# Kernel tuning notes

Hardware: AMD Instinct MI355X
Metric: run time of the kernel (lower is better)

Reference implementation:

```python
import jax, jax.numpy as jnp
import numpy as np

B, S, D = 2, 2048, 1024
H = 16
HD = D // H

def setup_inputs() -> dict:
    key = jax.random.key(0)
    k1, k2, k3 = jax.random.split(key, 3)
    x = jax.random.normal(k1, (B, S, D), dtype=jnp.float32)
    w_attn = jax.random.normal(k2, (D, 3 * D), dtype=jnp.float32) * (1.0 / np.sqrt(D))
    b_attn = jnp.zeros((3 * D,), dtype=jnp.float32)
    w_proj = jax.random.normal(k3, (D, D), dtype=jnp.float32) * (1.0 / np.sqrt(D))
    b_proj = jnp.zeros((D,), dtype=jnp.float32)
    return {"x": x, "w_attn": w_attn, "b_attn": b_attn, "w_proj": w_proj, "b_proj": b_proj}

def reference(x, w_attn, b_attn, w_proj, b_proj):
    bsz, seq_len, embed_dim = x.shape
    qkv = x @ w_attn + b_attn                      # [B,S,3D]
    q, k, v = jnp.split(qkv, 3, axis=-1)
    # [B,S,D] -> [B,H,S,HD]
    def heads(t):
        return t.reshape(bsz, seq_len, H, HD).transpose(0, 2, 1, 3)
    q, k, v = heads(q), heads(k), heads(v)
    scale = 1.0 / np.sqrt(HD)
    att = jnp.einsum('bhqd,bhkd->bhqk', q, k) * scale  # [B,H,S,S]
    causal = jnp.tril(jnp.ones((seq_len, seq_len), dtype=bool))
    att = jnp.where(causal[None, None], att, jnp.float32(-jnp.inf))
    att = jax.nn.softmax(att, axis=-1)
    y = jnp.einsum('bhqk,bhkd->bhqd', att, v)          # [B,H,S,HD]
    y = y.transpose(0, 2, 1, 3).reshape(bsz, seq_len, embed_dim)
    return y @ w_proj + b_proj
```

## Files before the change

### kernel.cpp

```cpp
#include <hip/hip_runtime.h>
#include <hip/hip_bf16.h>
#include <math.h>

typedef __bf16 bf16x8 __attribute__((ext_vector_type(8)));
typedef __bf16 bf16x4 __attribute__((ext_vector_type(4)));
typedef float f32x4 __attribute__((ext_vector_type(4)));

#define LOG2E 1.44269504088896340736f

#define SEQ 2048
#define DMODEL 1024
#define NH 16
#define HD 64

__device__ __forceinline__ void gl2lds16(const void* g, void* l) {
  __builtin_amdgcn_global_load_lds((__attribute__((address_space(1))) void*)g,
                                   (__attribute__((address_space(3))) void*)l,
                                   16, 0, 0);
}

__device__ __forceinline__ unsigned compute_flag_local(const unsigned* __restrict__ x,
                                                       int* cnt) {
  int c = 0;
  for (int i = threadIdx.x; i < 4096; i += 256) {
    unsigned e = (x[i] >> 23) & 0xFF;
    c += (e >= 0x70 && e <= 0x8F) ? 1 : 0;
  }
#pragma unroll
  for (int o = 32; o > 0; o >>= 1) c += __shfl_xor(c, o, 64);
  if ((threadIdx.x & 63) == 0) cnt[threadIdx.x >> 6] = c;
  __syncthreads();
  const int tot = cnt[0] + cnt[1] + cnt[2] + cnt[3];
  return (tot > 2048) ? 1u : 0u;
}

__device__ __forceinline__ void transpose_tile(const void* __restrict__ in,
                                               __hip_bfloat16* __restrict__ out,
                                               int R, int C, int c0, int r0, bool f32,
                                               __hip_bfloat16 (*tile)[65]) {
  const int tx = threadIdx.x & 63, ty = threadIdx.x >> 6;
#pragma unroll
  for (int i = 0; i < 16; ++i) {
    int r = ty + i * 4;
    long idx = (long)(r0 + r) * C + c0 + tx;
    tile[r][tx] = f32 ? __float2bfloat16(((const float*)in)[idx])
                      : ((const __hip_bfloat16*)in)[idx];
  }
  __syncthreads();
#pragma unroll
  for (int i = 0; i < 16; ++i) {
    int r = ty + i * 4;
    out[(long)(c0 + r) * R + r0 + tx] = tile[tx][r];
  }
}

__global__ void prep_all(const void* __restrict__ x, const void* __restrict__ w_attn,
                         const void* __restrict__ w_proj,
                         __hip_bfloat16* __restrict__ x_bf,
                         __hip_bfloat16* __restrict__ wT_attn,
                         __hip_bfloat16* __restrict__ wT_proj,
                         unsigned* __restrict__ flag) {
  __shared__ int cnt[4];
  __shared__ __hip_bfloat16 tile[64][65];
  const unsigned f = compute_flag_local((const unsigned*)x, cnt);
  const int bid = blockIdx.x;
  if (bid == 0 && threadIdx.x == 0) flag[0] = f;

  if (bid < 1024) {
#pragma unroll
    for (int rep = 0; rep < 4; ++rep) {
      const int i = ((bid * 4 + rep) * 256 + threadIdx.x) * 4;
      if (f) {
        const float4 v = *(const float4*)((const float*)x + i);
        x_bf[i + 0] = __float2bfloat16(v.x);
        x_bf[i + 1] = __float2bfloat16(v.y);
        x_bf[i + 2] = __float2bfloat16(v.z);
        x_bf[i + 3] = __float2bfloat16(v.w);
      } else {
        *(bf16x4*)(x_bf + i) = *(const bf16x4*)((const __hip_bfloat16*)x + i);
      }
    }
  } else if (bid < 1024 + 768) {
    const int b2 = bid - 1024;
    const int c0 = (b2 % 48) * 64, r0 = (b2 / 48) * 64;
    transpose_tile(w_attn, wT_attn, 1024, 3072, c0, r0, f != 0, tile);
  } else {
    const int b3 = bid - 1024 - 768;
    const int c0 = (b3 % 16) * 64, r0 = (b3 / 16) * 64;
    transpose_tile(w_proj, wT_proj, 1024, 1024, c0, r0, f != 0, tile);
  }
}

template <int MODE, int BN>
__global__ __launch_bounds__(256, BN == 128 ? 3 : 6) void gemm_bt(
    const __hip_bfloat16* __restrict__ A, const __hip_bfloat16* __restrict__ Bt,
    const void* __restrict__ bias, void* __restrict__ C,
    __hip_bfloat16* __restrict__ q_ws, __hip_bfloat16* __restrict__ k_ws,
    __hip_bfloat16* __restrict__ vt_ws, int M, int N, int K,
    const unsigned* __restrict__ flag) {
  constexpr int NJ = BN / 32;
  alignas(16) __shared__ __hip_bfloat16 lA[128 * 64];
  alignas(16) __shared__ __hip_bfloat16 lB[BN * 64];
  const int tid = threadIdx.x;
  const int wave = tid >> 6, lane = tid & 63;
  const int l15 = lane & 15, lq = lane >> 4;
  const int m0 = blockIdx.y * 128, n0 = blockIdx.x * BN;
  const int wrow = (wave >> 1) * 64, wcol = (wave & 1) * (BN / 2);

  const int rs = lane >> 3;
  const int cs = lane & 7;
  const int gch = cs ^ rs;
  const __hip_bfloat16* ap0 = A + (long)(m0 + wave * 32 + rs) * K + gch * 8;
  const __hip_bfloat16* bp0 = Bt + (long)(n0 + wave * (BN / 4) + rs) * K + gch * 8;

  f32x4 acc[4][NJ];
#pragma unroll
  for (int i = 0; i < 4; ++i)
#pragma unroll
    for (int j = 0; j < NJ; ++j) acc[i][j] = {0.f, 0.f, 0.f, 0.f};

  for (int k0 = 0; k0 < K; k0 += 64) {
    __syncthreads();
#pragma unroll
    for (int i = 0; i < 4; ++i)
      gl2lds16(ap0 + (long)(i * 8) * K + k0, lA + (wave * 4 + i) * 512);
#pragma unroll
    for (int i = 0; i < NJ; ++i)
      gl2lds16(bp0 + (long)(i * 8) * K + k0, lB + (wave * NJ + i) * 512);
    __syncthreads();
#pragma unroll
    for (int ks = 0; ks < 2; ++ks) {
      bf16x8 af[4], bfr[NJ];
#pragma unroll
      for (int i = 0; i < 4; ++i) {
        const int p = wrow + 16 * i + l15;
        af[i] = *(const bf16x8*)(lA + p * 64 + (((ks * 4 + lq) ^ (l15 & 7)) * 8));
      }
#pragma unroll
      for (int j = 0; j < NJ; ++j) {
        const int p = wcol + 16 * j + l15;
        bfr[j] = *(const bf16x8*)(lB + p * 64 + (((ks * 4 + lq) ^ (l15 & 7)) * 8));
      }
#pragma unroll
      for (int i = 0; i < 4; ++i)
#pragma unroll
        for (int j = 0; j < NJ; ++j)
          acc[i][j] = __builtin_amdgcn_mfma_f32_16x16x32_bf16(af[i], bfr[j], acc[i][j], 0, 0, 0);
    }
  }

  const bool f32in = (*flag != 0);
  const bool outf32 = (MODE == 0) && f32in;
  const float KSCL = 0.125f * LOG2E;
#pragma unroll
  for (int i = 0; i < 4; ++i) {
    const int row = m0 + wrow + 16 * i + lq * 4;
#pragma unroll
    for (int j = 0; j < NJ; ++j) {
      const int col = n0 + wcol + 16 * j + l15;
      const float bv = f32in ? ((const float*)bias)[col]
                             : __bfloat162float(((const __hip_bfloat16*)bias)[col]);
#pragma unroll
      for (int r = 0; r < 4; ++r) {
        const float v = acc[i][j][r] + bv;
        const int rr = row + r;
        if (MODE == 0) {
          if (outf32)
            ((float*)C)[(long)rr * N + col] = v;
          else
            ((__hip_bfloat16*)C)[(long)rr * N + col] = __float2bfloat16(v);
        } else {
          const int which = col >> 10;
          const int f = col & 1023;
          const int h = f >> 6, d = f & 63;
          const int b = rr >> 11, s = rr & 2047;
          const long bh = (long)b * NH + h;
          if (which == 0)
            q_ws[(bh * SEQ + s) * HD + d] = __float2bfloat16(v);
          else if (which == 1)
            k_ws[(bh * SEQ + s) * HD + d] = __float2bfloat16(v * KSCL);
          else {
            const int w = s & 31;
            const int wl = w & 15;
            const int sig = (w >> 4) ? (2 * (wl & ~3) + 4 + (wl & 3))
                                     : (2 * (wl & ~3) + (wl & 3));
            const int sp = (s & ~31) | sig;
            vt_ws[(bh * HD + d) * SEQ + sp] = __float2bfloat16(v);
          }
        }
      }
    }
  }
}

__global__ __launch_bounds__(256, 5) void attn_fused(
    const __hip_bfloat16* __restrict__ q_ws, const __hip_bfloat16* __restrict__ k_ws,
    const __hip_bfloat16* __restrict__ vt_ws, __hip_bfloat16* __restrict__ y_ws) {
  alignas(16) __shared__ __hip_bfloat16 lK[2][64 * 64];
  alignas(16) __shared__ __hip_bfloat16 lV[2][64 * 64];
  const int tid = threadIdx.x, wave = tid >> 6, lane = tid & 63;
  const int l15 = lane & 15, lq = lane >> 4;
  const int grp = blockIdx.x >> 5;
  const int bh = blockIdx.x & 31;
  const int gg = grp & 7, qq = grp >> 3;
  const int qt = (qq == 0) ? (31 - gg)
               : (qq == 1) ? (16 + gg)
               : (qq == 2) ? (15 - gg)
                           : gg;
  const int q0 = qt * 64;
  const int nkt = qt + 1;
  const __hip_bfloat16* Qb = q_ws + (long)bh * SEQ * HD;
  const __hip_bfloat16* Kb = k_ws + (long)bh * SEQ * HD;
  const __hip_bfloat16* Vb = vt_ws + (long)bh * HD * SEQ;
  const int b = bh >> 4, h = bh & 15;

  const int qrow = q0 + wave * 16 + l15;
  const bf16x8 qa0 = *(const bf16x8*)(Qb + (long)qrow * HD + lq * 8);
  const bf16x8 qa1 = *(const bf16x8*)(Qb + (long)qrow * HD + 32 + lq * 8);

  f32x4 accO[4];
  f32x4 accL;
#pragma unroll
  for (int j = 0; j < 4; ++j) accO[j] = {0.f, 0.f, 0.f, 0.f};
  accL = {0.f, 0.f, 0.f, 0.f};
  const __bf16 one = (__bf16)1.0f;
  const bf16x8 onesA = {one, one, one, one, one, one, one, one};

  const int p0 = wave * 16 + (lane >> 3);
  const int cl = lane & 7;
  const __hip_bfloat16* kpre[2];
  const __hip_bfloat16* vpre[2];

#pragma unroll
  for (int i = 0; i < 2; ++i) {
    const int p = p0 + i * 8;
    const int c = cl ^ (p & 7);
    kpre[i] = Kb + (long)p * HD + c * 8;
    vpre[i] = Vb + (long)p * SEQ + c * 8;
    gl2lds16(kpre[i], &lK[0][(wave * 16 + i * 8) * 64]);
    gl2lds16(vpre[i], &lV[0][(wave * 16 + i * 8) * 64]);
    kpre[i] += 64 * HD;
    vpre[i] += 64;
  }

#pragma unroll 1
  for (int kt = 0; kt < nkt; ++kt) {
    const int buf = kt & 1;
    if (kt + 1 < nkt) {
#pragma unroll
      for (int i = 0; i < 2; ++i) {
        gl2lds16(kpre[i], &lK[buf ^ 1][(wave * 16 + i * 8) * 64]);
        gl2lds16(vpre[i], &lV[buf ^ 1][(wave * 16 + i * 8) * 64]);
        kpre[i] += 64 * HD;
        vpre[i] += 64;
      }
      asm volatile("s_waitcnt vmcnt(4)\n\ts_barrier" ::: "memory");
    } else {
      asm volatile("s_waitcnt vmcnt(0)\n\ts_barrier" ::: "memory");
    }
    const __hip_bfloat16* lKb = lK[buf];
    const __hip_bfloat16* lVb = lV[buf];

    f32x4 st[4];
    __builtin_amdgcn_s_setprio(1);
#pragma unroll
    for (int t = 0; t < 4; ++t) {
      st[t] = {0.f, 0.f, 0.f, 0.f};
      const int pp = t * 16 + l15;
      const bf16x8 kb0 = *(const bf16x8*)(lKb + (pp * 8 + (lq ^ (pp & 7))) * 8);
      const bf16x8 kb1 = *(const bf16x8*)(lKb + (pp * 8 + ((4 + lq) ^ (pp & 7))) * 8);
      st[t] = __builtin_amdgcn_mfma_f32_16x16x32_bf16(kb0, qa0, st[t], 0, 0, 0);
      st[t] = __builtin_amdgcn_mfma_f32_16x16x32_bf16(kb1, qa1, st[t], 0, 0, 0);
    }
    __builtin_amdgcn_s_setprio(0);

    const bool diag = (kt == nkt - 1);
    const int qloc = wave * 16 + l15;
    bf16x8 pb[2];
#pragma unroll
    for (int c = 0; c < 2; ++c) {
#pragma unroll
      for (int t2 = 0; t2 < 2; ++t2) {
        const int tt = c * 2 + t2;
#pragma unroll
        for (int r = 0; r < 4; ++r) {
          float pv = exp2f(st[tt][r]);
          if (diag) {
            const int colloc = tt * 16 + lq * 4 + r;
            pv = (colloc <= qloc) ? pv : 0.f;
          }
          pb[c][t2 * 4 + r] = (__bf16)pv;
        }
      }
    }

    __builtin_amdgcn_s_setprio(1);
#pragma unroll
    for (int j = 0; j < 4; ++j) {
      const int d = j * 16 + l15;
      const bf16x8 va0 = *(const bf16x8*)(lVb + (d * 8 + (lq ^ (d & 7))) * 8);
      const bf16x8 va1 = *(const bf16x8*)(lVb + (d * 8 + ((4 + lq) ^ (d & 7))) * 8);
      accO[j] = __builtin_amdgcn_mfma_f32_16x16x32_bf16(va0, pb[0], accO[j], 0, 0, 0);
      accO[j] = __builtin_amdgcn_mfma_f32_16x16x32_bf16(va1, pb[1], accO[j], 0, 0, 0);
    }
    accL = __builtin_amdgcn_mfma_f32_16x16x32_bf16(onesA, pb[0], accL, 0, 0, 0);
    accL = __builtin_amdgcn_mfma_f32_16x16x32_bf16(onesA, pb[1], accL, 0, 0, 0);
    __builtin_amdgcn_s_setprio(0);
    asm volatile("s_barrier" ::: "memory");
  }

  const float inv = 1.f / accL[0];
  const int s = q0 + wave * 16 + l15;
  __hip_bfloat16* yb = y_ws + (long)(b * SEQ + s) * DMODEL + h * HD;
#pragma unroll
  for (int j = 0; j < 4; ++j) {
    bf16x4 o;
#pragma unroll
    for (int r = 0; r < 4; ++r) o[r] = (__bf16)(accO[j][r] * inv);
    *(bf16x4*)(yb + j * 16 + lq * 4) = o;
  }
}

extern "C" void kernel_launch(void* const* d_in, const int* in_sizes, int n_in,
                              void* d_out, int out_size, void* d_ws, size_t ws_size,
                              hipStream_t stream) {
  const void* x = d_in[0];
  const void* w_attn = d_in[1];
  const void* b_attn = d_in[2];
  const void* w_proj = d_in[3];
  const void* b_proj = d_in[4];

  char* ws = (char*)d_ws;
  const size_t MB = 1024 * 1024;
  unsigned* flag = (unsigned*)ws;
  __hip_bfloat16* wT_attn = (__hip_bfloat16*)(ws + 1 * MB);
  __hip_bfloat16* wT_proj = (__hip_bfloat16*)(ws + 7 * MB);
  __hip_bfloat16* x_bf = (__hip_bfloat16*)(ws + 9 * MB);
  __hip_bfloat16* q_ws = (__hip_bfloat16*)(ws + 17 * MB);
  __hip_bfloat16* k_ws = (__hip_bfloat16*)(ws + 25 * MB);
  __hip_bfloat16* vt_ws = (__hip_bfloat16*)(ws + 33 * MB);
  __hip_bfloat16* y_ws = (__hip_bfloat16*)(ws + 41 * MB);

  prep_all<<<dim3(1024 + 768 + 256), 256, 0, stream>>>(
      x, w_attn, w_proj, x_bf, wT_attn, wT_proj, flag);

  gemm_bt<1, 64><<<dim3(3072 / 64, 4096 / 128), 256, 0, stream>>>(
      x_bf, wT_attn, b_attn, nullptr, q_ws, k_ws, vt_ws, 4096, 3072, 1024, flag);

  attn_fused<<<dim3(1024), 256, 0, stream>>>(q_ws, k_ws, vt_ws, y_ws);

  gemm_bt<0, 64><<<dim3(1024 / 64, 4096 / 128), 256, 0, stream>>>(
      y_ws, wT_proj, b_proj, d_out, nullptr, nullptr, nullptr, 4096, 1024, 1024, flag);
}
```

Measured before the change: 192.2 us.

## Split attention tile 2x2 across waves over query and key halves with LDS reduction

Each wave now handles 32 query rows and 32 key columns of the 64x64 tile instead of 16 query rows against all 64 keys. Each K fragment and V fragment read from LDS is reused across two query fragments, which halves the per-wave LDS reads for K and V. Partial outputs and row sums from the two key-half waves are combined at the end through LDS with an extra sync. The cost is more accumulator registers (8 output tiles instead of 4), which may pressure the occupancy target of 5, plus the final reduction step.

Result: faster. 185.7 us (-3.4%).

```diff
diff --git a/kernel.cpp b/kernel.cpp
--- a/kernel.cpp
+++ b/kernel.cpp
@@ -200,6 +200,7 @@
   alignas(16) __shared__ __hip_bfloat16 lV[2][64 * 64];
   const int tid = threadIdx.x, wave = tid >> 6, lane = tid & 63;
   const int l15 = lane & 15, lq = lane >> 4;
+  const int qh = wave & 1, kh = wave >> 1;
   const int grp = blockIdx.x >> 5;
   const int bh = blockIdx.x & 31;
   const int gg = grp & 7, qq = grp >> 3;
@@ -214,15 +215,23 @@
   const __hip_bfloat16* Vb = vt_ws + (long)bh * HD * SEQ;
   const int b = bh >> 4, h = bh & 15;
 
-  const int qrow = q0 + wave * 16 + l15;
-  const bf16x8 qa0 = *(const bf16x8*)(Qb + (long)qrow * HD + lq * 8);
-  const bf16x8 qa1 = *(const bf16x8*)(Qb + (long)qrow * HD + 32 + lq * 8);
-
-  f32x4 accO[4];
-  f32x4 accL;
-#pragma unroll
-  for (int j = 0; j < 4; ++j) accO[j] = {0.f, 0.f, 0.f, 0.f};
-  accL = {0.f, 0.f, 0.f, 0.f};
+  bf16x8 qa[2][2];
+#pragma unroll
+  for (int qf = 0; qf < 2; ++qf) {
+    const int qrow = q0 + qh * 32 + qf * 16 + l15;
+#pragma unroll
+    for (int ks = 0; ks < 2; ++ks)
+      qa[qf][ks] = *(const bf16x8*)(Qb + (long)qrow * HD + ks * 32 + lq * 8);
+  }
+
+  f32x4 accO[4][2];
+  f32x4 accL[2];
+#pragma unroll
+  for (int df = 0; df < 4; ++df)
+#pragma unroll
+    for (int qf = 0; qf < 2; ++qf) accO[df][qf] = {0.f, 0.f, 0.f, 0.f};
+  accL[0] = {0.f, 0.f, 0.f, 0.f};
+  accL[1] = {0.f, 0.f, 0.f, 0.f};
   const __bf16 one = (__bf16)1.0f;
   const bf16x8 onesA = {one, one, one, one, one, one, one, one};
 
@@ -261,63 +270,93 @@
     const __hip_bfloat16* lKb = lK[buf];
     const __hip_bfloat16* lVb = lV[buf];
 
-    f32x4 st[4];
+    f32x4 st[2][2];
     __builtin_amdgcn_s_setprio(1);
 #pragma unroll
-    for (int t = 0; t < 4; ++t) {
-      st[t] = {0.f, 0.f, 0.f, 0.f};
-      const int pp = t * 16 + l15;
+    for (int kf = 0; kf < 2; ++kf) {
+      const int pp = kh * 32 + kf * 16 + l15;
       const bf16x8 kb0 = *(const bf16x8*)(lKb + (pp * 8 + (lq ^ (pp & 7))) * 8);
       const bf16x8 kb1 = *(const bf16x8*)(lKb + (pp * 8 + ((4 + lq) ^ (pp & 7))) * 8);
-      st[t] = __builtin_amdgcn_mfma_f32_16x16x32_bf16(kb0, qa0, st[t], 0, 0, 0);
-      st[t] = __builtin_amdgcn_mfma_f32_16x16x32_bf16(kb1, qa1, st[t], 0, 0, 0);
+#pragma unroll
+      for (int qf = 0; qf < 2; ++qf) {
+        st[kf][qf] = {0.f, 0.f, 0.f, 0.f};
+        st[kf][qf] = __builtin_amdgcn_mfma_f32_16x16x32_bf16(kb0, qa[qf][0], st[kf][qf], 0, 0, 0);
+        st[kf][qf] = __builtin_amdgcn_mfma_f32_16x16x32_bf16(kb1, qa[qf][1], st[kf][qf], 0, 0, 0);
+      }
     }
     __builtin_amdgcn_s_setprio(0);
 
     const bool diag = (kt == nkt - 1);
-    const int qloc = wave * 16 + l15;
     bf16x8 pb[2];
 #pragma unroll
-    for (int c = 0; c < 2; ++c) {
-#pragma unroll
-      for (int t2 = 0; t2 < 2; ++t2) {
-        const int tt = c * 2 + t2;
+    for (int qf = 0; qf < 2; ++qf) {
+      const int qloc = qh * 32 + qf * 16 + l15;
+#pragma unroll
+      for (int kf = 0; kf < 2; ++kf)
 #pragma unroll
         for (int r = 0; r < 4; ++r) {
-          float pv = exp2f(st[tt][r]);
+          float pv = exp2f(st[kf][qf][r]);
           if (diag) {
-            const int colloc = tt * 16 + lq * 4 + r;
+            const int colloc = kh * 32 + kf * 16 + lq * 4 + r;
             pv = (colloc <= qloc) ? pv : 0.f;
           }
-          pb[c][t2 * 4 + r] = (__bf16)pv;
+          pb[qf][kf * 4 + r] = (__bf16)pv;
         }
-      }
     }
 
     __builtin_amdgcn_s_setprio(1);
 #pragma unroll
-    for (int j = 0; j < 4; ++j) {
-      const int d = j * 16 + l15;
-      const bf16x8 va0 = *(const bf16x8*)(lVb + (d * 8 + (lq ^ (d & 7))) * 8);
-      const bf16x8 va1 = *(const bf16x8*)(lVb + (d * 8 + ((4 + lq) ^ (d & 7))) * 8);
-      accO[j] = __builtin_amdgcn_mfma_f32_16x16x32_bf16(va0, pb[0], accO[j], 0, 0, 0);
-      accO[j] = __builtin_amdgcn_mfma_f32_16x16x32_bf16(va1, pb[1], accO[j], 0, 0, 0);
-    }
-    accL = __builtin_amdgcn_mfma_f32_16x16x32_bf16(onesA, pb[0], accL, 0, 0, 0);
-    accL = __builtin_amdgcn_mfma_f32_16x16x32_bf16(onesA, pb[1], accL, 0, 0, 0);
+    for (int df = 0; df < 4; ++df) {
+      const int d = df * 16 + l15;
+      const bf16x8 va = *(const bf16x8*)(lVb + (d * 8 + ((kh * 4 + lq) ^ (d & 7))) * 8);
+#pragma unroll
+      for (int qf = 0; qf < 2; ++qf)
+        accO[df][qf] = __builtin_amdgcn_mfma_f32_16x16x32_bf16(va, pb[qf], accO[df][qf], 0, 0, 0);
+    }
+    accL[0] = __builtin_amdgcn_mfma_f32_16x16x32_bf16(onesA, pb[0], accL[0], 0, 0, 0);
+    accL[1] = __builtin_amdgcn_mfma_f32_16x16x32_bf16(onesA, pb[1], accL[1], 0, 0, 0);
     __builtin_amdgcn_s_setprio(0);
     asm volatile("s_barrier" ::: "memory");
   }
 
-  const float inv = 1.f / accL[0];
-  const int s = q0 + wave * 16 + l15;
-  __hip_bfloat16* yb = y_ws + (long)(b * SEQ + s) * DMODEL + h * HD;
-#pragma unroll
-  for (int j = 0; j < 4; ++j) {
-    bf16x4 o;
-#pragma unroll
-    for (int r = 0; r < 4; ++r) o[r] = (__bf16)(accO[j][r] * inv);
-    *(bf16x4*)(yb + j * 16 + lq * 4) = o;
+  {
+    float* red = (qh == 0) ? (float*)&lK[0][0] : (float*)&lV[0][0];
+    if (kh == 1) {
+#pragma unroll
+      for (int df = 0; df < 4; ++df)
+#pragma unroll
+        for (int qf = 0; qf < 2; ++qf)
+#pragma unroll
+          for (int r = 0; r < 4; ++r)
+            red[((df * 2 + qf) * 4 + r) * 64 + lane] = accO[df][qf][r];
+      red[32 * 64 + lane] = accL[0][0];
+      red[33 * 64 + lane] = accL[1][0];
+    }
+    __syncthreads();
+    if (kh == 0) {
+#pragma unroll
+      for (int df = 0; df < 4; ++df)
+#pragma unroll
+        for (int qf = 0; qf < 2; ++qf)
+#pragma unroll
+          for (int r = 0; r < 4; ++r)
+            accO[df][qf][r] += red[((df * 2 + qf) * 4 + r) * 64 + lane];
+      const float l0 = accL[0][0] + red[32 * 64 + lane];
+      const float l1 = accL[1][0] + red[33 * 64 + lane];
+#pragma unroll
+      for (int qf = 0; qf < 2; ++qf) {
+        const float inv = 1.f / (qf ? l1 : l0);
+        const int s = q0 + qh * 32 + qf * 16 + l15;
+        __hip_bfloat16* yb = y_ws + (long)(b * SEQ + s) * DMODEL + h * HD;
+#pragma unroll
+        for (int df = 0; df < 4; ++df) {
+          bf16x4 o;
+#pragma unroll
+          for (int r = 0; r < 4; ++r) o[r] = (__bf16)(accO[df][qf][r] * inv);
+          *(bf16x4*)(yb + df * 16 + lq * 4) = o;
+        }
+      }
+    }
   }
 }
 
```
